# Performance work log

Hardware: AMD Instinct MI355X
Metric: run time of the kernel (lower is better)

The kernel has to match this reference:

```python
import jax, jax.numpy as jnp
import numpy as np

# near_sym_b (13,19)-tap biorthogonal level-1 DTCWT filters (Kingsbury)
H0O = np.array([-0.0017578125, 0.0, 0.022265625, -0.046875, -0.0482421875,
                0.296875, 0.5554687500, 0.296875, -0.0482421875, -0.046875,
                0.022265625, 0.0, -0.0017578125], dtype=np.float32)
H1O = np.array([-7.0626e-05, 0.0, 1.34189e-03, -1.88341e-03, -7.15660e-03,
                2.38560e-02, 5.56431e-02, -5.16881e-02, -2.99758e-01,
                5.59431e-01, -2.99758e-01, -5.16881e-02, 5.56431e-02,
                2.38560e-02, -7.15660e-03, -1.88341e-03, 1.34189e-03,
                0.0, -7.0626e-05], dtype=np.float32)

def _alt(h):
    c = (len(h) - 1) // 2
    return (h * ((-1.0) ** (np.arange(len(h)) - c))).astype(np.float32)

G0O = _alt(H1O)  # synthesis lowpass  (PR complement of H1O)
G1O = _alt(H0O)  # synthesis highpass (PR complement of H0O)

DIM, HS, WS, BATCH, NB, BS = 64, 56, 56, 32, 4, 16


def _filt(x, h, axis):
    # depthwise 1D correlation with symmetric padding; x: (B,C,H,W), axis in {2,3}
    L = len(h); p = L // 2
    pad = [(0, 0)] * 4; pad[axis] = (p, p)
    xp = jnp.pad(x, pad, mode='symmetric')
    k = jnp.asarray(h, x.dtype).reshape((1, 1, L, 1) if axis == 2 else (1, 1, 1, L))
    B, C = x.shape[:2]
    y = jax.lax.conv_general_dilated(
        xp.reshape((B * C, 1) + xp.shape[2:]), k, (1, 1), 'VALID',
        dimension_numbers=('NCHW', 'OIHW', 'NCHW'))
    return y.reshape((B, C) + y.shape[2:])


def _q2c(y):
    y = y * np.float32(1.0 / np.sqrt(2.0))
    a = y[..., 0::2, 0::2]; b = y[..., 0::2, 1::2]
    c = y[..., 1::2, 0::2]; d = y[..., 1::2, 1::2]
    return (a - d, b + c), (a + d, b - c)


def _c2q(w1r, w1i, w2r, w2i):
    sc = np.float32(1.0 / np.sqrt(2.0))
    B, C, Hh, Wh = w1r.shape
    top = jnp.stack([(w1r + w2r) * sc, (w1i + w2i) * sc], axis=-1).reshape(B, C, Hh, 2 * Wh)
    bot = jnp.stack([(w1i - w2i) * sc, (w2r - w1r) * sc], axis=-1).reshape(B, C, Hh, 2 * Wh)
    return jnp.stack([top, bot], axis=3).reshape(B, C, 2 * Hh, 2 * Wh)


def dtcwt_fwd_j1(x):
    lo = _filt(x, H0O, 3); hi = _filt(x, H1O, 3)
    ll = _filt(lo, H0O, 2)
    (d15r, d15i), (d165r, d165i) = _q2c(_filt(lo, H1O, 2))   # LH -> 15/165 deg
    (d75r, d75i), (d105r, d105i) = _q2c(_filt(hi, H0O, 2))   # HL -> 75/105 deg
    (d45r, d45i), (d135r, d135i) = _q2c(_filt(hi, H1O, 2))   # HH -> 45/135 deg
    real = jnp.stack([d15r, d45r, d75r, d105r, d135r, d165r], axis=2)
    imag = jnp.stack([d15i, d45i, d75i, d105i, d135i, d165i], axis=2)
    return ll, jnp.stack([real, imag], axis=-1)  # (B,C,H,W), (B,C,6,H/2,W/2,2)


def dtcwt_inv_j1(ll, yh):
    r = yh[..., 0]; im = yh[..., 1]
    lh = _c2q(r[:, :, 0], im[:, :, 0], r[:, :, 5], im[:, :, 5])
    hl = _c2q(r[:, :, 2], im[:, :, 2], r[:, :, 3], im[:, :, 3])
    hh = _c2q(r[:, :, 1], im[:, :, 1], r[:, :, 4], im[:, :, 4])
    lo = _filt(ll, G0O, 2) + _filt(lh, G1O, 2)
    hi = _filt(hl, G0O, 2) + _filt(hh, G1O, 2)
    return _filt(lo, G0O, 3) + _filt(hi, G1O, 3)


def setup_inputs():
    key = jax.random.key(0)
    ks = jax.random.split(key, 6)
    return {
        'x': jax.random.normal(ks[0], (BATCH, HS * WS, DIM), jnp.float32),
        'w_ll': jax.random.normal(ks[1], (DIM, HS, WS), jnp.float32) * 0.02,
        'w1': jax.random.normal(ks[2], (2, NB, BS, BS), jnp.float32) * 0.02,
        'w2': jax.random.normal(ks[3], (2, NB, BS, BS), jnp.float32) * 0.02,
        'b1': jax.random.normal(ks[4], (2, NB, BS), jnp.float32) * 0.02,
        'b2': jax.random.normal(ks[5], (2, NB, BS), jnp.float32) * 0.02,
        'H': HS, 'W': WS,
    }


def reference(x, w_ll, w1, w2, b1, b2, H, W):
    Bt, N, C = x.shape
    xi = jnp.transpose(x.reshape(Bt, H, W, C), (0, 3, 1, 2)).astype(jnp.float32)
    xl, xh = dtcwt_fwd_j1(xi)
    xl = xl * w_ll                                  # (B,C,H,W) * (C,H,W)
    Hh, Wh = H // 2, W // 2
    # (B,C,6,Hh,Wh,2) -> (2,B,6,Hh,Wh,C) -> split C into (NB,BS) blocks
    xh = jnp.transpose(xh, (5, 0, 2, 3, 4, 1)).reshape(2, Bt, 6, Hh, Wh, NB, BS)
    xr, xim = xh[0], xh[1]
    mul = lambda t, w: jnp.einsum('...bd,bdk->...bk', t, w)
    r1 = jax.nn.relu(mul(xr, w1[0]) - mul(xim, w1[1]) + b1[0])
    i1 = jax.nn.relu(mul(xr, w1[1]) + mul(xim, w1[0]) + b1[1])
    r2 = mul(r1, w2[0]) - mul(i1, w2[1]) + b2[0]
    i2 = mul(r1, w2[1]) + mul(i1, w2[0]) + b2[1]
    xh2 = jnp.stack([r2, i2], axis=-1).reshape(Bt, 6, Hh, Wh, C, 2)
    xh2 = jnp.transpose(xh2, (0, 4, 1, 2, 3, 5))    # (B,C,6,Hh,Wh,2)
    y = dtcwt_inv_j1(xl, xh2)
    return jnp.transpose(y, (0, 2, 3, 1)).reshape(Bt, N, C)
```

## Files before the change

### kernel.cpp

```cpp
#include <hip/hip_runtime.h>

#define BT 32
#define CH 64
#define HS 56
#define WS 56
#define HH 28
#define WH 28

namespace {
constexpr float ISQ2 = 0.70710678118654752440f;
constexpr float F_H0[13] = {-0.0017578125f, 0.0f, 0.022265625f, -0.046875f,
    -0.0482421875f, 0.296875f, 0.55546875f, 0.296875f, -0.0482421875f,
    -0.046875f, 0.022265625f, 0.0f, -0.0017578125f};
constexpr float F_H1[19] = {-7.0626e-05f, 0.0f, 0.00134189f, -0.00188341f,
    -0.0071566f, 0.023856f, 0.0556431f, -0.0516881f, -0.299758f, 0.559431f,
    -0.299758f, -0.0516881f, 0.0556431f, 0.023856f, -0.0071566f,
    -0.00188341f, 0.00134189f, 0.0f, -7.0626e-05f};
constexpr float F_G0[19] = {7.0626e-05f, 0.0f, -0.00134189f, -0.00188341f,
    0.0071566f, 0.023856f, -0.0556431f, -0.0516881f, 0.299758f, 0.559431f,
    0.299758f, -0.0516881f, -0.0556431f, 0.023856f, 0.0071566f,
    -0.00188341f, -0.00134189f, 0.0f, 7.0626e-05f};
constexpr float F_G1[13] = {-0.0017578125f, 0.0f, 0.022265625f, 0.046875f,
    -0.0482421875f, -0.296875f, 0.55546875f, -0.296875f, -0.0482421875f,
    0.046875f, 0.022265625f, 0.0f, -0.0017578125f};
}

__device__ __forceinline__ int symi(int k) {
    k = (k < 0) ? (-1 - k) : k;
    k = (k >= HS) ? (2 * HS - 1 - k) : k;
    return k;
}

__device__ __forceinline__ unsigned short f2bf(float f) {
    unsigned u = __float_as_uint(f);
    u += 0x7fffu + ((u >> 16) & 1u);
    return (unsigned short)(u >> 16);
}
__device__ __forceinline__ float bf2f(unsigned short h) {
    return __uint_as_float(((unsigned)h) << 16);
}
__device__ __forceinline__ float2 bfp2(unsigned u) {
    float2 r;
    r.x = __uint_as_float((u & 0xffffu) << 16);
    r.y = __uint_as_float(u & 0xffff0000u);
    return r;
}
__device__ __forceinline__ unsigned packbf(float a, float b) {
    return (unsigned)f2bf(a) | ((unsigned)f2bf(b) << 16);
}

typedef __attribute__((ext_vector_type(8))) short short8;
typedef __attribute__((ext_vector_type(4))) float f32x4;

#define PPOS 784

__global__ __launch_bounds__(256) void k_wll_T(const float* __restrict__ wll,
                                               float* __restrict__ wllT) {
    __shared__ float tile[64][65];
    int pos0 = blockIdx.x * 64;
    int lp = threadIdx.x & 63, g = threadIdx.x >> 6;
#pragma unroll
    for (int r = 0; r < 16; ++r) {
        int cc = r * 4 + g;
        tile[cc][lp] = wll[cc * (HS * WS) + pos0 + lp];
    }
    __syncthreads();
#pragma unroll
    for (int r = 0; r < 16; ++r) {
        int pl = r * 4 + g;
        wllT[(pos0 + pl) * CH + lp] = tile[lp][pl];
    }
}

__global__ __launch_bounds__(256) void k_fwd_rows(const float* __restrict__ x,
                                                  unsigned short* __restrict__ lo,
                                                  unsigned short* __restrict__ hi) {
    int b = blockIdx.x / HS, h = blockIdx.x % HS;
    int strip = threadIdx.x >> 5;
    int c0 = (threadIdx.x & 31) * 2;
    int base = (b * HS + h) * WS * CH + c0;
    const float* row = x + base;
    unsigned short* lop = lo + base;
    unsigned short* hip = hi + base;
    int w0s = strip * 7;
    float Wa[19], Wb[19];
#pragma unroll
    for (int t = 0; t < 19; ++t) {
        float2 v = *(const float2*)(row + symi(w0s - 9 + t) * CH);
        Wa[t] = v.x; Wb[t] = v.y;
    }
    float2 nW[7];
#pragma unroll
    for (int u = 0; u < 7; ++u) nW[u] = *(const float2*)(row + symi(w0s + u + 10) * CH);
#pragma unroll
    for (int u = 0; u < 7; ++u) {
        int w = w0s + u;
        float aLo = 0.f, aHi = 0.f, bLo = 0.f, bHi = 0.f;
#pragma unroll
        for (int t = 0; t < 13; ++t) { aLo += F_H0[t] * Wa[3 + t]; bLo += F_H0[t] * Wb[3 + t]; }
#pragma unroll
        for (int t = 0; t < 19; ++t) { aHi += F_H1[t] * Wa[t]; bHi += F_H1[t] * Wb[t]; }
        *(unsigned*)(lop + w * CH) = packbf(aLo, bLo);
        *(unsigned*)(hip + w * CH) = packbf(aHi, bHi);
#pragma unroll
        for (int t = 0; t < 18; ++t) { Wa[t] = Wa[t + 1]; Wb[t] = Wb[t + 1]; }
        Wa[18] = nW[u].x; Wb[18] = nW[u].y;
    }
}

__global__ __launch_bounds__(256) void k_cols(
    const unsigned short* __restrict__ lo_in,
    const unsigned short* __restrict__ hi_in, const float* __restrict__ wllT,
    float* __restrict__ xl, unsigned short* __restrict__ sbT) {
    __shared__ float qT[2][4][64][9];
    int hq = blockIdx.y;
    int zmode = blockIdx.z;
    int b = blockIdx.x / WH, wp = blockIdx.x % WH;
    int w0 = 2 * wp, tid = threadIdx.x;
    int q = tid >> 6, c = tid & 63;
    int rp = q >> 1, jc = q & 1;
    const unsigned short* srcp = zmode ? hi_in : lo_in;
    const unsigned short* colbase = srcp + (b * HS) * WS * CH + (w0 + jc) * CH + c;
    {
        int hstart = 14 * hq + rp;
        float W[19];
#pragma unroll
        for (int t = 0; t < 19; ++t) W[t] = bf2f(colbase[symi(hstart - 9 + t) * (WS * CH)]);
        float nW0[7], nW1[7], nwll[7];
#pragma unroll
        for (int u = 0; u < 7; ++u) {
            int h = hstart + 2 * u;
            nW0[u] = bf2f(colbase[symi(h + 10) * (WS * CH)]);
            nW1[u] = bf2f(colbase[symi(h + 11) * (WS * CH)]);
        }
        if (zmode == 0) {
#pragma unroll
            for (int u = 0; u < 7; ++u)
                nwll[u] = wllT[((hstart + 2 * u) * WS + (w0 + jc)) * CH + c];
        }
#pragma unroll
        for (int u = 0; u < 7; ++u) {
            int h = hstart + 2 * u;
            float v0 = 0.f, v1 = 0.f;
#pragma unroll
            for (int t = 0; t < 13; ++t) v0 += F_H0[t] * W[3 + t];
#pragma unroll
            for (int t = 0; t < 19; ++t) v1 += F_H1[t] * W[t];
            if (zmode == 0) {
                xl[((b * HS + h) * WS + (w0 + jc)) * CH + c] = v0 * nwll[u];
                qT[0][q][c][u] = v1;
            } else {
                qT[0][q][c][u] = v0;
                qT[1][q][c][u] = v1;
            }
#pragma unroll
            for (int t = 0; t < 17; ++t) W[t] = W[t + 2];
            W[17] = nW0[u];
            W[18] = nW1[u];
        }
    }
    __syncthreads();
    {
        int qq = tid >> 5;
        int role = qq & 3, sub = qq >> 2;
        int c0 = (tid & 31) * 2;
        int rowA = role & 1, rowB = 3 - (role & 1);
        float sgn = (role == 1 || role == 2) ? 1.f : -1.f;
        int iL = sub * 4, iH = sub ? 7 : 4;
        int posb = wp * 28 + hq * 7;
        if (zmode == 0) {
            int p = (role < 2) ? role : role + 8;
            unsigned short* dst = sbT + ((p * BT + b) * PPOS + posb) * CH + c0;
            for (int ii = iL; ii < iH; ++ii) {
                float v0 = (qT[0][rowA][c0][ii] + sgn * qT[0][rowB][c0][ii]) * ISQ2;
                float v1 = (qT[0][rowA][c0 + 1][ii] + sgn * qT[0][rowB][c0 + 1][ii]) * ISQ2;
                *(unsigned*)(dst + ii * CH) = packbf(v0, v1);
            }
        } else {
#pragma unroll
            for (int src = 0; src < 2; ++src) {
                int p = (src == 0) ? (4 + role) : ((role < 2) ? (2 + role) : (6 + role));
                unsigned short* dst = sbT + ((p * BT + b) * PPOS + posb) * CH + c0;
                for (int ii = iL; ii < iH; ++ii) {
                    float v0 = (qT[src][rowA][c0][ii] + sgn * qT[src][rowB][c0][ii]) * ISQ2;
                    float v1 = (qT[src][rowA][c0 + 1][ii] + sgn * qT[src][rowB][c0 + 1][ii]) * ISQ2;
                    *(unsigned*)(dst + ii * CH) = packbf(v0, v1);
                }
            }
        }
    }
}

__global__ __launch_bounds__(64) void k_mix(
    const unsigned short* __restrict__ sbT, const float* __restrict__ w1,
    const float* __restrict__ w2, const float* __restrict__ b1,
    const float* __restrict__ b2, unsigned short* __restrict__ P0,
    unsigned short* __restrict__ P1, unsigned short* __restrict__ P2) {
    __shared__ unsigned short l1a[16][36];
    __shared__ unsigned short l1b[16][36];
    int blk = blockIdx.x;
    int pr = blk / (BT * 7);
    int rem = blk % (BT * 7);
    int b = rem / 7;
    int chunk = rem % 7;
    int nb = blockIdx.y;
    int sa = (pr == 0) ? 0 : (pr == 1) ? 2 : 1;
    int sb = (pr == 0) ? 5 : (pr == 1) ? 3 : 4;
    unsigned short* Pd = (pr == 0) ? P0 : (pr == 1) ? P1 : P2;
    int lane = threadIdx.x;
    int quad = lane >> 4;
    int n = lane & 15;

    short8 B1r, B1i, B2r, B2i;
#pragma unroll
    for (int j = 0; j < 8; ++j) {
        int kk = quad * 8 + j;
        int riw = kk >> 4, dd = kk & 15;
        float v1r = w1[nb * 256 + dd * 16 + n];
        float v1i = w1[1024 + nb * 256 + dd * 16 + n];
        float v2r = w2[nb * 256 + dd * 16 + n];
        float v2i = w2[1024 + nb * 256 + dd * 16 + n];
        B1r[j] = (short)f2bf(riw ? -v1i : v1r);
        B1i[j] = (short)f2bf(riw ? v1r : v1i);
        B2r[j] = (short)f2bf(riw ? -v2i : v2r);
        B2i[j] = (short)f2bf(riw ? v2r : v2i);
    }
    float bias1r = b1[nb * 16 + n], bias1i = b1[64 + nb * 16 + n];
    float bias2r = b2[nb * 16 + n], bias2i = b2[64 + nb * 16 + n];

    int rix = quad >> 1, dlo = (quad & 1) * 8;
    const unsigned short* pAa =
        sbT + (((sa * 2 + rix) * BT + b) * PPOS + n) * CH + nb * 16 + dlo;
    const unsigned short* pAb =
        sbT + (((sb * 2 + rix) * BT + b) * PPOS + n) * CH + nb * 16 + dlo;

    int pbase = chunk * 112;
    short8 A1a = *(const short8*)(pAa + pbase * CH);
    short8 A1b = *(const short8*)(pAb + pbase * CH);
    for (int t = 0; t < 7; ++t) {
        int pos0 = pbase + t * 16;
        short8 nAa = A1a, nAb = A1b;
        if (t < 6) {
            nAa = *(const short8*)(pAa + (pos0 + 16) * CH);
            nAb = *(const short8*)(pAb + (pos0 + 16) * CH);
        }
        f32x4 a1r = {bias1r, bias1r, bias1r, bias1r};
        f32x4 a1i = {bias1i, bias1i, bias1i, bias1i};
        f32x4 b1r_ = a1r, b1i_ = a1i;
        a1r = __builtin_amdgcn_mfma_f32_16x16x32_bf16(A1a, B1r, a1r, 0, 0, 0);
        a1i = __builtin_amdgcn_mfma_f32_16x16x32_bf16(A1a, B1i, a1i, 0, 0, 0);
        b1r_ = __builtin_amdgcn_mfma_f32_16x16x32_bf16(A1b, B1r, b1r_, 0, 0, 0);
        b1i_ = __builtin_amdgcn_mfma_f32_16x16x32_bf16(A1b, B1i, b1i_, 0, 0, 0);
#pragma unroll
        for (int r = 0; r < 4; ++r) {
            int pos = quad * 4 + r;
            l1a[pos][n] = f2bf(fmaxf(a1r[r], 0.f));
            l1a[pos][16 + n] = f2bf(fmaxf(a1i[r], 0.f));
            l1b[pos][n] = f2bf(fmaxf(b1r_[r], 0.f));
            l1b[pos][16 + n] = f2bf(fmaxf(b1i_[r], 0.f));
        }
        union { short8 s8; uint2 u2[2]; } a2a, a2b;
        const unsigned short* rowpa = &l1a[n][0];
        const unsigned short* rowpb = &l1b[n][0];
        a2a.u2[0] = *(const uint2*)(rowpa + quad * 8);
        a2a.u2[1] = *(const uint2*)(rowpa + quad * 8 + 4);
        a2b.u2[0] = *(const uint2*)(rowpb + quad * 8);
        a2b.u2[1] = *(const uint2*)(rowpb + quad * 8 + 4);
        f32x4 aAr = {bias2r, bias2r, bias2r, bias2r};
        f32x4 aAi = {bias2i, bias2i, bias2i, bias2i};
        f32x4 aBr = aAr, aBi = aAi;
        aAr = __builtin_amdgcn_mfma_f32_16x16x32_bf16(a2a.s8, B2r, aAr, 0, 0, 0);
        aAi = __builtin_amdgcn_mfma_f32_16x16x32_bf16(a2a.s8, B2i, aAi, 0, 0, 0);
        aBr = __builtin_amdgcn_mfma_f32_16x16x32_bf16(a2b.s8, B2r, aBr, 0, 0, 0);
        aBi = __builtin_amdgcn_mfma_f32_16x16x32_bf16(a2b.s8, B2i, aBi, 0, 0, 0);
#pragma unroll
        for (int r = 0; r < 4; ++r) {
            int pos_g = pos0 + quad * 4 + r;
            int wp = pos_g / 28, ii = pos_g - wp * 28;
            int o = ((b * HS + 2 * ii) * WS + 2 * wp) * CH + nb * 16 + n;
            Pd[o] = f2bf((aAr[r] + aBr[r]) * ISQ2);
            Pd[o + CH] = f2bf((aAi[r] + aBi[r]) * ISQ2);
            Pd[o + WS * CH] = f2bf((aAi[r] - aBi[r]) * ISQ2);
            Pd[o + WS * CH + CH] = f2bf((aBr[r] - aAr[r]) * ISQ2);
        }
        A1a = nAa; A1b = nAb;
    }
}

template <int MODE>
__device__ __forceinline__ void inv_cols_body(
    const float* __restrict__ xl, const unsigned short* __restrict__ P0,
    const unsigned short* __restrict__ P1, const unsigned short* __restrict__ P2,
    float* __restrict__ lo2, float* __restrict__ hi2) {
    int hf = blockIdx.y;
    int b = blockIdx.x / 7, wg = blockIdx.x % 7;
    int wl = threadIdx.x >> 5, l = threadIdx.x & 31;
    int c0 = l * 2;
    int w = wg * 8 + wl;
    int base = (b * HS) * WS * CH + w * CH + c0;
    const int st = WS * CH;
    const unsigned short* Bp = (MODE == 0) ? P0 : P2;
    float* outp = (MODE == 0) ? lo2 : hi2;
    auto ldA = [&](int r) -> float2 {
        if (MODE == 0) return *(const float2*)(xl + base + r * st);
        return bfp2(*(const unsigned*)(P1 + base + r * st));
    };
    auto ldB = [&](int r) -> float2 {
        return bfp2(*(const unsigned*)(Bp + base + r * st));
    };
    int h0 = hf * 14;
    float Aa[19], Ab[19], Ba[13], Bb[13];
#pragma unroll
    for (int t = 0; t < 19; ++t) { float2 v = ldA(symi(h0 - 9 + t)); Aa[t] = v.x; Ab[t] = v.y; }
#pragma unroll
    for (int t = 0; t < 13; ++t) { float2 v = ldB(symi(h0 - 6 + t)); Ba[t] = v.x; Bb[t] = v.y; }
    int hg = h0;
#pragma unroll
    for (int g = 0; g < 4; ++g) {
        const int cnt = (g < 3) ? 4 : 2;
        float2 nA[4], nB[4];
#pragma unroll
        for (int u = 0; u < cnt; ++u) nA[u] = ldA(symi(hg + u + 10));
#pragma unroll
        for (int u = 0; u < cnt; ++u) nB[u] = ldB(symi(hg + u + 7));
#pragma unroll
        for (int u = 0; u < cnt; ++u) {
            int h = hg + u;
            float acca = 0.f, accb = 0.f;
#pragma unroll
            for (int t = 0; t < 19; ++t) { acca += F_G0[t] * Aa[t]; accb += F_G0[t] * Ab[t]; }
#pragma unroll
            for (int t = 0; t < 13; ++t) { acca += F_G1[t] * Ba[t]; accb += F_G1[t] * Bb[t]; }
            float2 ov; ov.x = acca; ov.y = accb;
            *(float2*)(outp + base + h * st) = ov;
#pragma unroll
            for (int t = 0; t < 18; ++t) { Aa[t] = Aa[t + 1]; Ab[t] = Ab[t + 1]; }
#pragma unroll
            for (int t = 0; t < 12; ++t) { Ba[t] = Ba[t + 1]; Bb[t] = Bb[t + 1]; }
            Aa[18] = nA[u].x; Ab[18] = nA[u].y;
            Ba[12] = nB[u].x; Bb[12] = nB[u].y;
        }
        hg += cnt;
    }
}

__global__ __launch_bounds__(256) void k_inv_cols(
    const float* __restrict__ xl, const unsigned short* __restrict__ P0,
    const unsigned short* __restrict__ P1, const unsigned short* __restrict__ P2,
    float* __restrict__ lo2, float* __restrict__ hi2) {
    if (blockIdx.z == 0)
        inv_cols_body<0>(xl, P0, P1, P2, lo2, hi2);
    else
        inv_cols_body<1>(xl, P0, P1, P2, lo2, hi2);
}

__global__ __launch_bounds__(256) void k_inv_rows(const float* __restrict__ lo2,
                                                  const float* __restrict__ hi2,
                                                  float* __restrict__ out) {
    int b = blockIdx.x / HS, h = blockIdx.x % HS;
    int strip = threadIdx.x >> 5;
    int c0 = (threadIdx.x & 31) * 2;
    int base = (b * HS + h) * WS * CH + c0;
    const float* rlo = lo2 + base;
    const float* rhi = hi2 + base;
    float* op = out + base;
    int w0s = strip * 7;
    float Aa[19], Ab[19], Ba[13], Bb[13];
#pragma unroll
    for (int t = 0; t < 19; ++t) {
        float2 v = *(const float2*)(rlo + symi(w0s - 9 + t) * CH);
        Aa[t] = v.x; Ab[t] = v.y;
    }
#pragma unroll
    for (int t = 0; t < 13; ++t) {
        float2 v = *(const float2*)(rhi + symi(w0s - 6 + t) * CH);
        Ba[t] = v.x; Bb[t] = v.y;
    }
    float2 nA[7], nB[7];
#pragma unroll
    for (int u = 0; u < 7; ++u) nA[u] = *(const float2*)(rlo + symi(w0s + u + 10) * CH);
#pragma unroll
    for (int u = 0; u < 7; ++u) nB[u] = *(const float2*)(rhi + symi(w0s + u + 7) * CH);
#pragma unroll
    for (int u = 0; u < 7; ++u) {
        int w = w0s + u;
        float acca = 0.f, accb = 0.f;
#pragma unroll
        for (int t = 0; t < 19; ++t) { acca += F_G0[t] * Aa[t]; accb += F_G0[t] * Ab[t]; }
#pragma unroll
        for (int t = 0; t < 13; ++t) { acca += F_G1[t] * Ba[t]; accb += F_G1[t] * Bb[t]; }
        float2 ov; ov.x = acca; ov.y = accb;
        *(float2*)(op + w * CH) = ov;
#pragma unroll
        for (int t = 0; t < 18; ++t) { Aa[t] = Aa[t + 1]; Ab[t] = Ab[t + 1]; }
#pragma unroll
        for (int t = 0; t < 12; ++t) { Ba[t] = Ba[t + 1]; Bb[t] = Bb[t + 1]; }
        Aa[18] = nA[u].x; Ab[18] = nA[u].y;
        Ba[12] = nB[u].x; Bb[12] = nB[u].y;
    }
}

extern "C" void kernel_launch(void* const* d_in, const int* in_sizes, int n_in,
                              void* d_out, int out_size, void* d_ws, size_t ws_size,
                              hipStream_t stream) {
    const float* x = (const float*)d_in[0];
    const float* w_ll = (const float*)d_in[1];
    const float* w1 = (const float*)d_in[2];
    const float* w2 = (const float*)d_in[3];
    const float* b1 = (const float*)d_in[4];
    const float* b2 = (const float*)d_in[5];
    float* out = (float*)d_out;

    const size_t A = (size_t)BT * HS * WS * CH;
    const size_t SBf = (size_t)12 * 64 * BT * PPOS / 2;
    float* wsf = (float*)d_ws;
    float* xl = wsf;
    unsigned short* sbT = (unsigned short*)(wsf + A);
    float* lo2 = wsf + A;
    float* hi2 = wsf + A + SBf;
    unsigned short* lo_in = (unsigned short*)(wsf + A + SBf + A);
    unsigned short* hi_in = lo_in + A;
    unsigned short* P0 = hi_in + A;
    unsigned short* P1 = P0 + A;
    unsigned short* P2 = P1 + A;

    float* wllT = out;

    k_wll_T<<<49, 256, 0, stream>>>(w_ll, wllT);
    k_fwd_rows<<<BT * HS, 256, 0, stream>>>(x, lo_in, hi_in);
    k_cols<<<dim3(BT * WH, 4, 2), 256, 0, stream>>>(lo_in, hi_in, wllT, xl, sbT);
    k_mix<<<dim3(3 * BT * 7, 4), 64, 0, stream>>>(sbT, w1, w2, b1, b2, P0, P1, P2);
    k_inv_cols<<<dim3(BT * 7, 4, 2), 256, 0, stream>>>(xl, P0, P1, P2, lo2, hi2);
    k_inv_rows<<<BT * HS, 256, 0, stream>>>(lo2, hi2, out);
}
```

Baseline: 182.9 us.

## Lengthen column strips, merge mix blocks, double-buffer inverse column loads

The forward column kernel and the inverse column kernel now give each thread twice as many output rows. This halves the grid and the redundant halo reloads of the 19-tap and 13-tap windows. The mix kernel folds the four channel blocks into one 256-thread block, one wave per block, with per-wave LDS staging. The inverse column loop now prefetches the next row group into alternating register buffers while computing the current one. The cost is higher register pressure, which may lower occupancy, and fewer blocks to spread across the GPU.

```diff
diff --git a/kernel.cpp b/kernel.cpp
--- a/kernel.cpp
+++ b/kernel.cpp
@@ -112,8 +112,8 @@
     const unsigned short* __restrict__ lo_in,
     const unsigned short* __restrict__ hi_in, const float* __restrict__ wllT,
     float* __restrict__ xl, unsigned short* __restrict__ sbT) {
-    __shared__ float qT[2][4][64][9];
-    int hq = blockIdx.y;
+    __shared__ float qT[2][4][64][15];
+    int hf = blockIdx.y;
     int zmode = blockIdx.z;
     int b = blockIdx.x / WH, wp = blockIdx.x % WH;
     int w0 = 2 * wp, tid = threadIdx.x;
@@ -122,24 +122,24 @@
     const unsigned short* srcp = zmode ? hi_in : lo_in;
     const unsigned short* colbase = srcp + (b * HS) * WS * CH + (w0 + jc) * CH + c;
     {
-        int hstart = 14 * hq + rp;
+        int hstart = 2 * (hf * 14) + rp;
         float W[19];
 #pragma unroll
         for (int t = 0; t < 19; ++t) W[t] = bf2f(colbase[symi(hstart - 9 + t) * (WS * CH)]);
-        float nW0[7], nW1[7], nwll[7];
-#pragma unroll
-        for (int u = 0; u < 7; ++u) {
+        float nW0[14], nW1[14], nwll[14];
+#pragma unroll
+        for (int u = 0; u < 14; ++u) {
             int h = hstart + 2 * u;
             nW0[u] = bf2f(colbase[symi(h + 10) * (WS * CH)]);
             nW1[u] = bf2f(colbase[symi(h + 11) * (WS * CH)]);
         }
         if (zmode == 0) {
 #pragma unroll
-            for (int u = 0; u < 7; ++u)
+            for (int u = 0; u < 14; ++u)
                 nwll[u] = wllT[((hstart + 2 * u) * WS + (w0 + jc)) * CH + c];
         }
 #pragma unroll
-        for (int u = 0; u < 7; ++u) {
+        for (int u = 0; u < 14; ++u) {
             int h = hstart + 2 * u;
             float v0 = 0.f, v1 = 0.f;
 #pragma unroll
@@ -162,28 +162,39 @@
     __syncthreads();
     {
         int qq = tid >> 5;
-        int role = qq & 3, sub = qq >> 2;
+        int role = qq & 3, half = qq >> 2;
         int c0 = (tid & 31) * 2;
         int rowA = role & 1, rowB = 3 - (role & 1);
         float sgn = (role == 1 || role == 2) ? 1.f : -1.f;
-        int iL = sub * 4, iH = sub ? 7 : 4;
-        int posb = wp * 28 + hq * 7;
+        int posb = wp * 28 + hf * 14;
         if (zmode == 0) {
             int p = (role < 2) ? role : role + 8;
+            const float* qA0 = &qT[0][rowA][c0][0];
+            const float* qA1 = &qT[0][rowA][c0 + 1][0];
+            const float* qB0 = &qT[0][rowB][c0][0];
+            const float* qB1 = &qT[0][rowB][c0 + 1][0];
             unsigned short* dst = sbT + ((p * BT + b) * PPOS + posb) * CH + c0;
-            for (int ii = iL; ii < iH; ++ii) {
-                float v0 = (qT[0][rowA][c0][ii] + sgn * qT[0][rowB][c0][ii]) * ISQ2;
-                float v1 = (qT[0][rowA][c0 + 1][ii] + sgn * qT[0][rowB][c0 + 1][ii]) * ISQ2;
+#pragma unroll
+            for (int g = 0; g < 7; ++g) {
+                int ii = half * 7 + g;
+                float v0 = (qA0[ii] + sgn * qB0[ii]) * ISQ2;
+                float v1 = (qA1[ii] + sgn * qB1[ii]) * ISQ2;
                 *(unsigned*)(dst + ii * CH) = packbf(v0, v1);
             }
         } else {
 #pragma unroll
             for (int src = 0; src < 2; ++src) {
                 int p = (src == 0) ? (4 + role) : ((role < 2) ? (2 + role) : (6 + role));
+                const float* qA0 = &qT[src][rowA][c0][0];
+                const float* qA1 = &qT[src][rowA][c0 + 1][0];
+                const float* qB0 = &qT[src][rowB][c0][0];
+                const float* qB1 = &qT[src][rowB][c0 + 1][0];
                 unsigned short* dst = sbT + ((p * BT + b) * PPOS + posb) * CH + c0;
-                for (int ii = iL; ii < iH; ++ii) {
-                    float v0 = (qT[src][rowA][c0][ii] + sgn * qT[src][rowB][c0][ii]) * ISQ2;
-                    float v1 = (qT[src][rowA][c0 + 1][ii] + sgn * qT[src][rowB][c0 + 1][ii]) * ISQ2;
+#pragma unroll
+                for (int g = 0; g < 7; ++g) {
+                    int ii = half * 7 + g;
+                    float v0 = (qA0[ii] + sgn * qB0[ii]) * ISQ2;
+                    float v1 = (qA1[ii] + sgn * qB1[ii]) * ISQ2;
                     *(unsigned*)(dst + ii * CH) = packbf(v0, v1);
                 }
             }
@@ -191,23 +202,25 @@
     }
 }
 
-__global__ __launch_bounds__(64) void k_mix(
+__global__ __launch_bounds__(256) void k_mix(
     const unsigned short* __restrict__ sbT, const float* __restrict__ w1,
     const float* __restrict__ w2, const float* __restrict__ b1,
     const float* __restrict__ b2, unsigned short* __restrict__ P0,
     unsigned short* __restrict__ P1, unsigned short* __restrict__ P2) {
-    __shared__ unsigned short l1a[16][36];
-    __shared__ unsigned short l1b[16][36];
+    __shared__ unsigned short l1a[4][16][36];
+    __shared__ unsigned short l1b[4][16][36];
     int blk = blockIdx.x;
     int pr = blk / (BT * 7);
     int rem = blk % (BT * 7);
     int b = rem / 7;
     int chunk = rem % 7;
-    int nb = blockIdx.y;
     int sa = (pr == 0) ? 0 : (pr == 1) ? 2 : 1;
     int sb = (pr == 0) ? 5 : (pr == 1) ? 3 : 4;
     unsigned short* Pd = (pr == 0) ? P0 : (pr == 1) ? P1 : P2;
-    int lane = threadIdx.x;
+    int tid = threadIdx.x;
+    int lane = tid & 63;
+    int wv = tid >> 6;
+    int nb = __builtin_amdgcn_readfirstlane(wv);
     int quad = lane >> 4;
     int n = lane & 15;
 
@@ -254,14 +267,14 @@
 #pragma unroll
         for (int r = 0; r < 4; ++r) {
             int pos = quad * 4 + r;
-            l1a[pos][n] = f2bf(fmaxf(a1r[r], 0.f));
-            l1a[pos][16 + n] = f2bf(fmaxf(a1i[r], 0.f));
-            l1b[pos][n] = f2bf(fmaxf(b1r_[r], 0.f));
-            l1b[pos][16 + n] = f2bf(fmaxf(b1i_[r], 0.f));
+            l1a[wv][pos][n] = f2bf(fmaxf(a1r[r], 0.f));
+            l1a[wv][pos][16 + n] = f2bf(fmaxf(a1i[r], 0.f));
+            l1b[wv][pos][n] = f2bf(fmaxf(b1r_[r], 0.f));
+            l1b[wv][pos][16 + n] = f2bf(fmaxf(b1i_[r], 0.f));
         }
         union { short8 s8; uint2 u2[2]; } a2a, a2b;
-        const unsigned short* rowpa = &l1a[n][0];
-        const unsigned short* rowpb = &l1b[n][0];
+        const unsigned short* rowpa = &l1a[wv][n][0];
+        const unsigned short* rowpb = &l1b[wv][n][0];
         a2a.u2[0] = *(const uint2*)(rowpa + quad * 8);
         a2a.u2[1] = *(const uint2*)(rowpa + quad * 8 + 4);
         a2b.u2[0] = *(const uint2*)(rowpb + quad * 8);
@@ -308,40 +321,53 @@
     auto ldB = [&](int r) -> float2 {
         return bfp2(*(const unsigned*)(Bp + base + r * st));
     };
-    int h0 = hf * 14;
+    int h0 = hf * 28;
     float Aa[19], Ab[19], Ba[13], Bb[13];
 #pragma unroll
     for (int t = 0; t < 19; ++t) { float2 v = ldA(symi(h0 - 9 + t)); Aa[t] = v.x; Ab[t] = v.y; }
 #pragma unroll
     for (int t = 0; t < 13; ++t) { float2 v = ldB(symi(h0 - 6 + t)); Ba[t] = v.x; Bb[t] = v.y; }
-    int hg = h0;
-#pragma unroll
-    for (int g = 0; g < 4; ++g) {
-        const int cnt = (g < 3) ? 4 : 2;
-        float2 nA[4], nB[4];
-#pragma unroll
-        for (int u = 0; u < cnt; ++u) nA[u] = ldA(symi(hg + u + 10));
-#pragma unroll
-        for (int u = 0; u < cnt; ++u) nB[u] = ldB(symi(hg + u + 7));
-#pragma unroll
-        for (int u = 0; u < cnt; ++u) {
-            int h = hg + u;
-            float acca = 0.f, accb = 0.f;
-#pragma unroll
-            for (int t = 0; t < 19; ++t) { acca += F_G0[t] * Aa[t]; accb += F_G0[t] * Ab[t]; }
-#pragma unroll
-            for (int t = 0; t < 13; ++t) { acca += F_G1[t] * Ba[t]; accb += F_G1[t] * Bb[t]; }
-            float2 ov; ov.x = acca; ov.y = accb;
-            *(float2*)(outp + base + h * st) = ov;
-#pragma unroll
-            for (int t = 0; t < 18; ++t) { Aa[t] = Aa[t + 1]; Ab[t] = Ab[t + 1]; }
-#pragma unroll
-            for (int t = 0; t < 12; ++t) { Ba[t] = Ba[t + 1]; Bb[t] = Bb[t + 1]; }
-            Aa[18] = nA[u].x; Ab[18] = nA[u].y;
-            Ba[12] = nB[u].x; Bb[12] = nB[u].y;
-        }
-        hg += cnt;
-    }
+    float2 pa0[4], pb0[4], pa1[4], pb1[4];
+#define LDG(bA, bB, G)                                                          \
+    {                                                                           \
+        _Pragma("unroll") for (int u = 0; u < 4; ++u)                           \
+            bA[u] = ldA(symi(h0 + (G) * 4 + u + 10));                           \
+        _Pragma("unroll") for (int u = 0; u < 4; ++u)                           \
+            bB[u] = ldB(symi(h0 + (G) * 4 + u + 7));                            \
+    }
+#define CPG(bA, bB, G)                                                          \
+    {                                                                           \
+        _Pragma("unroll") for (int u = 0; u < 4; ++u) {                         \
+            int h = h0 + (G) * 4 + u;                                           \
+            float acca = 0.f, accb = 0.f;                                       \
+            _Pragma("unroll") for (int t = 0; t < 19; ++t) {                    \
+                acca += F_G0[t] * Aa[t]; accb += F_G0[t] * Ab[t];               \
+            }                                                                   \
+            _Pragma("unroll") for (int t = 0; t < 13; ++t) {                    \
+                acca += F_G1[t] * Ba[t]; accb += F_G1[t] * Bb[t];               \
+            }                                                                   \
+            float2 ov; ov.x = acca; ov.y = accb;                                \
+            *(float2*)(outp + base + h * st) = ov;                              \
+            _Pragma("unroll") for (int t = 0; t < 18; ++t) {                    \
+                Aa[t] = Aa[t + 1]; Ab[t] = Ab[t + 1];                           \
+            }                                                                   \
+            _Pragma("unroll") for (int t = 0; t < 12; ++t) {                    \
+                Ba[t] = Ba[t + 1]; Bb[t] = Bb[t + 1];                           \
+            }                                                                   \
+            Aa[18] = bA[u].x; Ab[18] = bA[u].y;                                 \
+            Ba[12] = bB[u].x; Bb[12] = bB[u].y;                                 \
+        }                                                                       \
+    }
+    LDG(pa0, pb0, 0) LDG(pa1, pb1, 1)
+    CPG(pa0, pb0, 0) LDG(pa0, pb0, 2)
+    CPG(pa1, pb1, 1) LDG(pa1, pb1, 3)
+    CPG(pa0, pb0, 2) LDG(pa0, pb0, 4)
+    CPG(pa1, pb1, 3) LDG(pa1, pb1, 5)
+    CPG(pa0, pb0, 4) LDG(pa0, pb0, 6)
+    CPG(pa1, pb1, 5)
+    CPG(pa0, pb0, 6)
+#undef LDG
+#undef CPG
 }
 
 __global__ __launch_bounds__(256) void k_inv_cols(
@@ -428,8 +454,8 @@
 
     k_wll_T<<<49, 256, 0, stream>>>(w_ll, wllT);
     k_fwd_rows<<<BT * HS, 256, 0, stream>>>(x, lo_in, hi_in);
-    k_cols<<<dim3(BT * WH, 4, 2), 256, 0, stream>>>(lo_in, hi_in, wllT, xl, sbT);
-    k_mix<<<dim3(3 * BT * 7, 4), 64, 0, stream>>>(sbT, w1, w2, b1, b2, P0, P1, P2);
-    k_inv_cols<<<dim3(BT * 7, 4, 2), 256, 0, stream>>>(xl, P0, P1, P2, lo2, hi2);
+    k_cols<<<dim3(BT * WH, 2, 2), 256, 0, stream>>>(lo_in, hi_in, wllT, xl, sbT);
+    k_mix<<<3 * BT * 7, 256, 0, stream>>>(sbT, w1, w2, b1, b2, P0, P1, P2);
+    k_inv_cols<<<dim3(BT * 7, 2, 2), 256, 0, stream>>>(xl, P0, P1, P2, lo2, hi2);
     k_inv_rows<<<BT * HS, 256, 0, stream>>>(lo2, hi2, out);
 }
```

New measurement: 178.6 us. -2.3%, faster.
